# Kernel optimization log

Measured on AMD Instinct MI355X. Metric: run time of the kernel, lower is better.

## Reference

```python
import jax, jax.numpy as jnp
from jax import lax
import numpy as np

B, S, D, H, OUT = 32, 512, 512, 512, 256


def setup_inputs() -> dict:
    key = jax.random.key(0)
    ks = jax.random.split(key, 12)
    sc = 0.05
    return {
        "x": jax.random.normal(ks[0], (B, S, D), jnp.float32),
        "Wf0": jax.random.normal(ks[1], (D + H, H), jnp.float32) * sc,
        "bf0": jax.random.normal(ks[2], (H,), jnp.float32) * sc,
        "Wb0": jax.random.normal(ks[3], (D + H, H), jnp.float32) * sc,
        "bb0": jax.random.normal(ks[4], (H,), jnp.float32) * sc,
        "Wf1": jax.random.normal(ks[5], (3 * H, H), jnp.float32) * sc,
        "bf1": jax.random.normal(ks[6], (H,), jnp.float32) * sc,
        "Wb1": jax.random.normal(ks[7], (3 * H, H), jnp.float32) * sc,
        "bb1": jax.random.normal(ks[8], (H,), jnp.float32) * sc,
        "Wfc": jax.random.normal(ks[9], (2 * H, OUT), jnp.float32) * sc,
        "bfc": jax.random.normal(ks[10], (OUT,), jnp.float32) * sc,
    }


def _direction(xin, W, b, reverse):
    # xin: [B,S,Din]; W: [Din+H, H]. Split into input and hidden parts so the
    # big input projection is one GEMM; only h @ Wh stays in the scan.
    Din = xin.shape[-1]
    Wx, Wh = W[:Din], W[Din:]
    xw = jnp.einsum('bsd,dh->sbh', xin, Wx) + b  # [S,B,H]

    def step(h, xt):
        h = jnp.tanh(xt + h @ Wh)
        return h, h

    h0 = jnp.zeros((xin.shape[0], Wh.shape[1]), xin.dtype)
    h_last, ys = lax.scan(step, h0, xw, reverse=reverse)
    return h_last, jnp.transpose(ys, (1, 0, 2))  # [B,S,H]


def _bilayer(xin, Wf, bf, Wb, bb):
    h_f, out_f = _direction(xin, Wf, bf, reverse=False)
    h_b, out_b = _direction(xin, Wb, bb, reverse=True)
    return jnp.concatenate([out_f, out_b], axis=-1), h_f, h_b


def reference(x, Wf0, bf0, Wb0, bb0, Wf1, bf1, Wb1, bb1, Wfc, bfc):
    y0, hf0, hb0 = _bilayer(x, Wf0, bf0, Wb0, bb0)
    y1, hf1, hb1 = _bilayer(y0, Wf1, bf1, Wb1, bb1)
    seq_repr = jnp.concatenate([hf1, hb1], axis=-1)  # [B, 2H]
    logits = seq_repr @ Wfc + bfc
    final_hf = jnp.stack([hf0, hf1])  # [L,B,H]
    final_hb = jnp.stack([hb0, hb1])
    return logits, final_hf, final_hb
```

## Files before the change

### kernel.cpp

```cpp
#include <hip/hip_runtime.h>


typedef unsigned short u16;
typedef unsigned int u32;
typedef __attribute__((ext_vector_type(8))) short short8;
typedef __attribute__((ext_vector_type(4))) float f32x4;
typedef __attribute__((ext_vector_type(2))) unsigned int u32x2;

#define DEV static __device__ __forceinline__

DEV u16 f2bf(float f) {
  u32 u = __builtin_bit_cast(u32, f);
  u = (u + 0x7fffu + ((u >> 16) & 1u)) >> 16;
  return (u16)u;
}
DEV float bf2f(u16 h) { return __builtin_bit_cast(float, ((u32)h) << 16); }

DEV f32x4 MFMA(short8 a, short8 b, f32x4 c) {
  return __builtin_amdgcn_mfma_f32_16x16x32_bf16(a, b, c, 0, 0, 0);
}

DEV float fast_tanh(float x) {
  float e = exp2f(x * 2.885390082f);
  return 1.0f - 2.0f * __builtin_amdgcn_rcpf(e + 1.0f);
}

DEV short8 ld_b128_coh(const u16* p) {
  short8 r;
  asm volatile("global_load_dwordx4 %0, %1, off sc0 sc1" : "=v"(r) : "v"(p) : "memory");
  return r;
}
DEV short8 ld_b128_l2(const u16* p) {
  short8 r;
  asm volatile("global_load_dwordx4 %0, %1, off sc0" : "=v"(r) : "v"(p) : "memory");
  return r;
}
DEV f32x4 ld_f32x4_vm(const float* p) {
  f32x4 r;
  asm volatile("global_load_dwordx4 %0, %1, off" : "=v"(r) : "v"(p) : "memory");
  return r;
}
DEV u32 ld_u32_coh(const u32* p) {
  u32 r;
  asm volatile("global_load_dword %0, %1, off sc0 sc1\n\ts_waitcnt vmcnt(0)"
               : "=v"(r) : "v"(p) : "memory");
  return r;
}
DEV void st_b64_coh(u16* p, u32x2 v) {
  asm volatile("global_store_dwordx2 %0, %1, off sc0 sc1" :: "v"(p), "v"(v) : "memory");
}
DEV void st_b64_l2(u16* p, u32x2 v) {
  asm volatile("global_store_dwordx2 %0, %1, off sc0" :: "v"(p), "v"(v) : "memory");
}
DEV void st_u32_coh(u32* p, u32 v) {
  asm volatile("global_store_dword %0, %1, off sc0 sc1" :: "v"(p), "v"(v) : "memory");
}
DEV void vm_drain() { asm volatile("s_waitcnt vmcnt(0)" ::: "memory"); }

template<bool LOCAL>
DEV u32 tag_poll(u32* p) {
  u32 r; u32 z = 0;
  if (LOCAL)
    asm volatile("global_atomic_add %0, %1, %2, off sc0\n\ts_waitcnt vmcnt(0)"
                 : "=v"(r) : "v"(p), "v"(z) : "memory");
  else
    asm volatile("global_atomic_add %0, %1, %2, off sc0 sc1\n\ts_waitcnt vmcnt(0)"
                 : "=v"(r) : "v"(p), "v"(z) : "memory");
  return r;
}
template<bool LOCAL>
DEV void tag_post(u32* p) {
  u32 one = 1;
  if (LOCAL)
    asm volatile("global_atomic_add %0, %1, off" :: "v"(p), "v"(one) : "memory");
  else
    asm volatile("global_atomic_add %0, %1, off sc1" :: "v"(p), "v"(one) : "memory");
}

constexpr size_t OFF_CNT  = 0;
constexpr size_t OFF_MB   = 1024;
constexpr size_t OFF_WT0F = 32768;
constexpr size_t NE_WT0   = 512 * 1024;
constexpr size_t SZ_WT0   = NE_WT0 * 2 * 2;
constexpr size_t OFF_WT0B = OFF_WT0F + SZ_WT0;
constexpr size_t OFF_WT1F = OFF_WT0B + SZ_WT0;
constexpr size_t NE_WT1   = 512 * 1536;
constexpr size_t SZ_WT1   = NE_WT1 * 2 * 2;
constexpr size_t OFF_WT1B = OFF_WT1F + SZ_WT1;
constexpr size_t OFF_XWF  = OFF_WT1B + SZ_WT1;
constexpr size_t SZ_XW    = 16384ull * 512 * 4;
constexpr size_t OFF_XWB  = OFF_XWF + SZ_XW;
constexpr size_t OFF_Y0   = OFF_XWB + SZ_XW;
constexpr size_t SZ_Y0    = 16384ull * 1024 * 4;
constexpr size_t OFF_H    = OFF_Y0 + SZ_Y0;

DEV void phase_barrier(u32* c, u32 target) {
  __syncthreads();
  if (threadIdx.x == 0) {
    __hip_atomic_fetch_add(c, 1u, __ATOMIC_RELEASE, __HIP_MEMORY_SCOPE_AGENT);
    int spins = 0;
    while (__hip_atomic_load(c, __ATOMIC_RELAXED, __HIP_MEMORY_SCOPE_AGENT) < target) {
      if (spins < 16) __builtin_amdgcn_s_sleep(32);
      else { __builtin_amdgcn_s_sleep(127); __builtin_amdgcn_s_sleep(127); }
      if (++spins > (1 << 20)) break;
    }
    __builtin_amdgcn_fence(__ATOMIC_ACQUIRE, "agent");
  }
  __syncthreads();
}

DEV void proj_phase(const float* __restrict__ A, bool perm, int bpitch, int bkoff, int K,
                    const u16* __restrict__ wfh, const u16* __restrict__ wfl,
                    const u16* __restrict__ wbh, const u16* __restrict__ wbl,
                    const float* __restrict__ biasF, const float* __restrict__ biasB,
                    float* __restrict__ Cf, float* __restrict__ Cb,
                    u16* aHi, u16* aLo, u16* bHi, u16* bLo) {
  const int tid = threadIdx.x;
  const int l = tid & 63, w = tid >> 6;
  const int lr = l & 15, lk = (l >> 4) * 8;
  const int wm = (w >> 1) * 64, wn = (w & 1) * 64;
  for (int t = blockIdx.x; t < 1024; t += 256) {
    const int dir = t >> 9, tile = t & 511;
    const int mbase = (tile >> 2) * 128, nbase = (tile & 3) * 128;
    const u16* bh_src = dir ? wbh : wfh;
    const u16* bl_src = dir ? wbl : wfl;
    const float* bias = dir ? biasB : biasF;
    float* C = dir ? Cb : Cf;
    f32x4 acc[4][4] = {};
    for (int kk = 0; kk < K; kk += 32) {
      {
        const int row = tid >> 1, half = tid & 1;
        const int r = mbase + row;
        const int srcRow = perm ? (((r & 31) << 9) + (r >> 5)) : r;
        const float* ap = A + (size_t)srcRow * K + kk + half * 16;
        f32x4 q0 = *(const f32x4*)(ap + 0);
        f32x4 q1 = *(const f32x4*)(ap + 4);
        f32x4 q2 = *(const f32x4*)(ap + 8);
        f32x4 q3 = *(const f32x4*)(ap + 12);
        short8 h0, l0, h1, l1;
        #pragma unroll
        for (int e = 0; e < 4; ++e) {
          { float v = q0[e]; u16 hv = f2bf(v); h0[e]   = (short)hv; l0[e]   = (short)f2bf(v - bf2f(hv)); }
          { float v = q1[e]; u16 hv = f2bf(v); h0[e+4] = (short)hv; l0[e+4] = (short)f2bf(v - bf2f(hv)); }
          { float v = q2[e]; u16 hv = f2bf(v); h1[e]   = (short)hv; l1[e]   = (short)f2bf(v - bf2f(hv)); }
          { float v = q3[e]; u16 hv = f2bf(v); h1[e+4] = (short)hv; l1[e+4] = (short)f2bf(v - bf2f(hv)); }
        }
        const int o = row * 40 + half * 16;
        *(short8*)&aHi[o] = h0; *(short8*)&aHi[o + 8] = h1;
        *(short8*)&aLo[o] = l0; *(short8*)&aLo[o + 8] = l1;
        const size_t bo = (size_t)(nbase + row) * bpitch + bkoff + kk + half * 16;
        *(short8*)&bHi[o]     = *(const short8*)&bh_src[bo];
        *(short8*)&bHi[o + 8] = *(const short8*)&bh_src[bo + 8];
        *(short8*)&bLo[o]     = *(const short8*)&bl_src[bo];
        *(short8*)&bLo[o + 8] = *(const short8*)&bl_src[bo + 8];
      }
      __syncthreads();
      short8 afh[4], afl[4], bfh[4], bfl[4];
      #pragma unroll
      for (int i = 0; i < 4; ++i) {
        afh[i] = *(short8*)&aHi[(wm + i * 16 + lr) * 40 + lk];
        afl[i] = *(short8*)&aLo[(wm + i * 16 + lr) * 40 + lk];
        bfh[i] = *(short8*)&bHi[(wn + i * 16 + lr) * 40 + lk];
        bfl[i] = *(short8*)&bLo[(wn + i * 16 + lr) * 40 + lk];
      }
      #pragma unroll
      for (int i = 0; i < 4; ++i)
        #pragma unroll
        for (int j = 0; j < 4; ++j) {
          acc[i][j] = MFMA(afh[i], bfh[j], acc[i][j]);
          acc[i][j] = MFMA(afh[i], bfl[j], acc[i][j]);
          acc[i][j] = MFMA(afl[i], bfh[j], acc[i][j]);
        }
      __syncthreads();
    }
    #pragma unroll
    for (int i = 0; i < 4; ++i)
      #pragma unroll
      for (int j = 0; j < 4; ++j) {
        const int gcol = nbase + wn + j * 16 + lr;
        const float bv = bias[gcol];
        #pragma unroll
        for (int rr = 0; rr < 4; ++rr) {
          const int grow = mbase + wm + i * 16 + (l >> 4) * 4 + rr;
          C[(size_t)grow * 512 + gcol] = acc[i][j][rr] + bv;
        }
      }
  }
}

template<bool LOCAL>
DEV void recurrence(bool fwd, const float* __restrict__ xw,
                    const u16* __restrict__ wtHi, const u16* __restrict__ wtLo,
                    int wpitch, int wkoff,
                    u16* __restrict__ hHi, u16* __restrict__ hLo,
                    float* __restrict__ y0, int ycol0,
                    u32* mb, int wgslot, float* red) {
  const int tid = threadIdx.x;
  const int l = tid & 63, w = tid >> 6;
  const int lr = l & 15, lk4 = l >> 4;
  const int c0 = wgslot * 64;
  short8 wfh[4][4], wfl[4][4];
  #pragma unroll
  for (int ct = 0; ct < 4; ++ct)
    #pragma unroll
    for (int ks = 0; ks < 4; ++ks) {
      const size_t o = (size_t)(c0 + ct * 16 + lr) * wpitch + wkoff + w * 128 + ks * 32 + lk4 * 8;
      wfh[ct][ks] = *(const short8*)&wtHi[o];
      wfl[ct][ks] = *(const short8*)&wtLo[o];
    }
  const int frow = (w & 1) * 16 + lr;
  const int fcb  = c0 + (w >> 1) * 16 + lk4 * 4;
  const u32 mySlot = (u32)(wgslot * 4 + w);
  u32* pollp = mb + wgslot * 64 + (l & 31);
  int budget = 1 << 22;
  for (int t = 0; t < 512; ++t) {
    const int s = fwd ? t : (511 - t);
    const float* xwp = xw + (size_t)(s * 32 + frow) * 512 + fcb;
    f32x4 xwA = ld_f32x4_vm(xwp);
    f32x4 xwB = ld_f32x4_vm(xwp + 32);
    if (t) {
      for (;;) {
        u32 v = tag_poll<LOCAL>(pollp);
        if (__all((int)(v >= (u32)t))) break;
        if (--budget < 0) break;
      }
    }
    const u16* hh = hHi + (t & 1) * 16384;
    const u16* hl = hLo + (t & 1) * 16384;
    u16* nhh = hHi + ((t & 1) ^ 1) * 16384;
    u16* nhl = hLo + ((t & 1) ^ 1) * 16384;
    short8 hfh0[4], hfl0[4], hfh1[4], hfl1[4];
    #pragma unroll
    for (int g = 0; g < 4; ++g) {
      const int k = w * 128 + g * 32 + lk4 * 8;
      if (LOCAL) {
        hfh0[g] = ld_b128_l2(&hh[lr * 512 + k]);
        hfl0[g] = ld_b128_l2(&hl[lr * 512 + k]);
        hfh1[g] = ld_b128_l2(&hh[(16 + lr) * 512 + k]);
        hfl1[g] = ld_b128_l2(&hl[(16 + lr) * 512 + k]);
      } else {
        hfh0[g] = ld_b128_coh(&hh[lr * 512 + k]);
        hfl0[g] = ld_b128_coh(&hl[lr * 512 + k]);
        hfh1[g] = ld_b128_coh(&hh[(16 + lr) * 512 + k]);
        hfl1[g] = ld_b128_coh(&hl[(16 + lr) * 512 + k]);
      }
    }
    f32x4 acc[4][2] = {};
    #pragma unroll
    for (int g = 0; g < 4; ++g) {
      if (g == 0)      asm volatile("s_waitcnt vmcnt(12)" ::: "memory");
      else if (g == 1) asm volatile("s_waitcnt vmcnt(8)"  ::: "memory");
      else if (g == 2) asm volatile("s_waitcnt vmcnt(4)"  ::: "memory");
      else             asm volatile("s_waitcnt vmcnt(0)"  ::: "memory");
      __builtin_amdgcn_sched_barrier(0);
      #pragma unroll
      for (int ct = 0; ct < 4; ++ct) {
        acc[ct][0] = MFMA(wfh[ct][g], hfh0[g], acc[ct][0]);
        acc[ct][0] = MFMA(wfh[ct][g], hfl0[g], acc[ct][0]);
        acc[ct][0] = MFMA(wfl[ct][g], hfh0[g], acc[ct][0]);
        acc[ct][1] = MFMA(wfh[ct][g], hfh1[g], acc[ct][1]);
        acc[ct][1] = MFMA(wfh[ct][g], hfl1[g], acc[ct][1]);
        acc[ct][1] = MFMA(wfl[ct][g], hfh1[g], acc[ct][1]);
      }
    }
    #pragma unroll
    for (int ct = 0; ct < 4; ++ct)
      #pragma unroll
      for (int rh = 0; rh < 2; ++rh)
        *(f32x4*)&red[((w * 8 + ct * 2 + rh) * 64 + l) * 4] = acc[ct][rh];
    __syncthreads();
    f32x4 finA = xwA, finB = xwB;
    #pragma unroll
    for (int wp = 0; wp < 4; ++wp) {
      finA += *(const f32x4*)&red[((wp * 8 + w) * 64 + l) * 4];
      finB += *(const f32x4*)&red[((wp * 8 + w + 4) * 64 + l) * 4];
    }
    f32x4 tA, tB;
    #pragma unroll
    for (int rr = 0; rr < 4; ++rr) { tA[rr] = fast_tanh(finA[rr]); tB[rr] = fast_tanh(finB[rr]); }
    u32x2 hwA, lwA, hwB, lwB;
    {
      u16 hv[8], lv[8];
      #pragma unroll
      for (int i = 0; i < 4; ++i) {
        hv[i] = f2bf(tA[i]); lv[i] = f2bf(tA[i] - bf2f(hv[i]));
        hv[4 + i] = f2bf(tB[i]); lv[4 + i] = f2bf(tB[i] - bf2f(hv[4 + i]));
      }
      hwA[0] = (u32)hv[0] | ((u32)hv[1] << 16); hwA[1] = (u32)hv[2] | ((u32)hv[3] << 16);
      lwA[0] = (u32)lv[0] | ((u32)lv[1] << 16); lwA[1] = (u32)lv[2] | ((u32)lv[3] << 16);
      hwB[0] = (u32)hv[4] | ((u32)hv[5] << 16); hwB[1] = (u32)hv[6] | ((u32)hv[7] << 16);
      lwB[0] = (u32)lv[4] | ((u32)lv[5] << 16); lwB[1] = (u32)lv[6] | ((u32)lv[7] << 16);
    }
    if (LOCAL) {
      st_b64_l2(&nhh[frow * 512 + fcb], hwA);
      st_b64_l2(&nhl[frow * 512 + fcb], lwA);
      st_b64_l2(&nhh[frow * 512 + fcb + 32], hwB);
      st_b64_l2(&nhl[frow * 512 + fcb + 32], lwB);
    } else {
      st_b64_coh(&nhh[frow * 512 + fcb], hwA);
      st_b64_coh(&nhl[frow * 512 + fcb], lwA);
      st_b64_coh(&nhh[frow * 512 + fcb + 32], hwB);
      st_b64_coh(&nhl[frow * 512 + fcb + 32], lwB);
    }
    vm_drain();
    if (l < 8) tag_post<LOCAL>(mb + l * 64 + mySlot);
    if (y0) {
      *(f32x4*)&y0[(size_t)(s * 32 + frow) * 1024 + ycol0 + fcb] = tA;
      *(f32x4*)&y0[(size_t)(s * 32 + frow) * 1024 + ycol0 + fcb + 32] = tB;
    }
  }
}

__global__ void rnn_init(u32* c) {
  #pragma unroll
  for (int i = 0; i < 8; ++i) c[threadIdx.x * 8 + i] = 0;
}

__global__ __launch_bounds__(256, 1) void rnn_main(
    const float* __restrict__ x,
    const float* __restrict__ Wf0, const float* __restrict__ bf0,
    const float* __restrict__ Wb0, const float* __restrict__ bb0,
    const float* __restrict__ Wf1, const float* __restrict__ bf1,
    const float* __restrict__ Wb1, const float* __restrict__ bb1,
    const float* __restrict__ Wfc, const float* __restrict__ bfc,
    float* __restrict__ out, char* __restrict__ ws) {
  __shared__ __align__(16) u16 lds[20480];
  u16* aHi = lds; u16* aLo = lds + 5120; u16* bHi = lds + 10240; u16* bLo = lds + 15360;
  float* red = (float*)lds;
  __shared__ u32 sh_xcd, sh_slot, sh_el;

  u32* cnt = (u32*)(ws + OFF_CNT);
  u32* mbase = (u32*)(ws + OFF_MB);
  u16* wt0f_hi = (u16*)(ws + OFF_WT0F); u16* wt0f_lo = wt0f_hi + NE_WT0;
  u16* wt0b_hi = (u16*)(ws + OFF_WT0B); u16* wt0b_lo = wt0b_hi + NE_WT0;
  u16* wt1f_hi = (u16*)(ws + OFF_WT1F); u16* wt1f_lo = wt1f_hi + NE_WT1;
  u16* wt1b_hi = (u16*)(ws + OFF_WT1B); u16* wt1b_lo = wt1b_hi + NE_WT1;
  float* xwf = (float*)(ws + OFF_XWF);
  float* xwb = (float*)(ws + OFF_XWB);
  float* y0  = (float*)(ws + OFF_Y0);
  u16* hb = (u16*)(ws + OFF_H);

  const int gtid = blockIdx.x * 256 + threadIdx.x;
  const int bid = blockIdx.x;

  if (threadIdx.x == 0) {
    u32 xcd;
    asm volatile("s_getreg_b32 %0, hwreg(HW_REG_XCC_ID)" : "=s"(xcd));
    xcd &= 7u;
    sh_xcd = xcd;
    sh_slot = __hip_atomic_fetch_add(&cnt[128 + xcd], 1u, __ATOMIC_RELAXED,
                                     __HIP_MEMORY_SCOPE_AGENT);
  }
  __syncthreads();
  const u32 myXcd = sh_xcd, mySlotIdx = sh_slot;

  for (u32 j = gtid; j < (u32)NE_WT0; j += 65536u) {
    const u32 n = j >> 10, r = j & 1023;
    float v = Wf0[(size_t)r * 512 + n];
    u16 hv = f2bf(v); wt0f_hi[j] = hv; wt0f_lo[j] = f2bf(v - bf2f(hv));
    v = Wb0[(size_t)r * 512 + n];
    hv = f2bf(v); wt0b_hi[j] = hv; wt0b_lo[j] = f2bf(v - bf2f(hv));
  }
  for (u32 j = gtid; j < (u32)NE_WT1; j += 65536u) {
    const u32 n = j / 1536u, r = j - n * 1536u;
    float v = Wf1[(size_t)r * 512 + n];
    u16 hv = f2bf(v); wt1f_hi[j] = hv; wt1f_lo[j] = f2bf(v - bf2f(hv));
    v = Wb1[(size_t)r * 512 + n];
    hv = f2bf(v); wt1b_hi[j] = hv; wt1b_lo[j] = f2bf(v - bf2f(hv));
  }
  for (u32 j = gtid; j < 131072u; j += 65536u) ((u32*)hb)[j] = 0;

  u32 ep = 0;
  phase_barrier(cnt, (++ep) * 256);

  if (bid == 0 && threadIdx.x == 0) {
    u32 cv[8];
    for (int i = 0; i < 8; ++i) cv[i] = ld_u32_coh(&cnt[128 + i]);
    int fwdX = 0;
    for (int i = 1; i < 8; ++i) if (cv[i] > cv[fwdX]) fwdX = i;
    int bwdX = (fwdX == 0) ? 1 : 0;
    for (int i = 0; i < 8; ++i) if (i != fwdX && cv[i] > cv[bwdX]) bwdX = i;
    u32 ok = (cv[fwdX] >= 8 && cv[bwdX] >= 8) ? 1u : 0u;
    st_u32_coh(&cnt[160], (u32)fwdX | ((u32)bwdX << 4) | (ok << 8));
    vm_drain();
  }
  phase_barrier(cnt, (++ep) * 256);
  if (threadIdx.x == 0) sh_el = ld_u32_coh(&cnt[160]);
  __syncthreads();
  const u32 el = sh_el;
  const int fwdX = (int)(el & 15), bwdX = (int)((el >> 4) & 15);
  const bool useLocal = ((el >> 8) & 1) != 0;

  bool rf, rb; int slot;
  if (useLocal) {
    rf = ((int)myXcd == fwdX) && (mySlotIdx < 8);
    rb = ((int)myXcd == bwdX) && (mySlotIdx < 8);
    slot = (int)mySlotIdx;
  } else {
    rf = bid < 8;
    rb = bid >= 8 && bid < 16;
    slot = bid & 7;
  }

  proj_phase(x, true, 1024, 0, 512, wt0f_hi, wt0f_lo, wt0b_hi, wt0b_lo,
             bf0, bb0, xwf, xwb, aHi, aLo, bHi, bLo);
  phase_barrier(cnt, (++ep) * 256);

  if (rf) {
    if (useLocal) recurrence<true >(true,  xwf, wt0f_hi, wt0f_lo, 1024, 512,
                    hb + 0 * 65536, hb + 0 * 65536 + 32768, y0, 0,   mbase,        slot, red);
    else          recurrence<false>(true,  xwf, wt0f_hi, wt0f_lo, 1024, 512,
                    hb + 0 * 65536, hb + 0 * 65536 + 32768, y0, 0,   mbase,        slot, red);
  } else if (rb) {
    if (useLocal) recurrence<true >(false, xwb, wt0b_hi, wt0b_lo, 1024, 512,
                    hb + 1 * 65536, hb + 1 * 65536 + 32768, y0, 512, mbase + 1024, slot, red);
    else          recurrence<false>(false, xwb, wt0b_hi, wt0b_lo, 1024, 512,
                    hb + 1 * 65536, hb + 1 * 65536 + 32768, y0, 512, mbase + 1024, slot, red);
  }
  phase_barrier(cnt, (++ep) * 256);

  proj_phase(y0, false, 1536, 0, 1024, wt1f_hi, wt1f_lo, wt1b_hi, wt1b_lo,
             bf1, bb1, xwf, xwb, aHi, aLo, bHi, bLo);
  phase_barrier(cnt, (++ep) * 256);

  if (rf) {
    if (useLocal) recurrence<true >(true,  xwf, wt1f_hi, wt1f_lo, 1536, 1024,
                    hb + 2 * 65536, hb + 2 * 65536 + 32768, nullptr, 0, mbase + 2048, slot, red);
    else          recurrence<false>(true,  xwf, wt1f_hi, wt1f_lo, 1536, 1024,
                    hb + 2 * 65536, hb + 2 * 65536 + 32768, nullptr, 0, mbase + 2048, slot, red);
  } else if (rb) {
    if (useLocal) recurrence<true >(false, xwb, wt1b_hi, wt1b_lo, 1536, 1024,
                    hb + 3 * 65536, hb + 3 * 65536 + 32768, nullptr, 0, mbase + 3072, slot, red);
    else          recurrence<false>(false, xwb, wt1b_hi, wt1b_lo, 1536, 1024,
                    hb + 3 * 65536, hb + 3 * 65536 + 32768, nullptr, 0, mbase + 3072, slot, red);
  }
  phase_barrier(cnt, (++ep) * 256);

  {
    const int i = gtid;
    const int dl = i >> 14, idx = i & 16383;
    const u16* hh = hb + dl * 65536;
    const u16* hl = hh + 32768;
    const float v = bf2f(hh[idx]) + bf2f(hl[idx]);
    const int base = 8192 + ((dl & 1) ? 32768 : 0) + ((dl >> 1) ? 16384 : 0);
    out[base + idx] = v;
  }
  if (bid < 32) {
    const int gid = gtid;
    const int b = gid >> 8, o = gid & 255;
    const u16* f1h = hb + 2 * 65536; const u16* f1l = f1h + 32768;
    const u16* b1h = hb + 3 * 65536; const u16* b1l = b1h + 32768;
    float a = bfc[o];
    for (int k = 0; k < 512; ++k)
      a += (bf2f(f1h[b * 512 + k]) + bf2f(f1l[b * 512 + k])) * Wfc[(size_t)k * 256 + o];
    for (int k = 0; k < 512; ++k)
      a += (bf2f(b1h[b * 512 + k]) + bf2f(b1l[b * 512 + k])) * Wfc[(size_t)(512 + k) * 256 + o];
    out[gid] = a;
  }
}

extern "C" void kernel_launch(void* const* d_in, const int* in_sizes, int n_in,
                              void* d_out, int out_size, void* d_ws, size_t ws_size,
                              hipStream_t stream) {
  (void)in_sizes; (void)n_in; (void)out_size; (void)ws_size;
  const float* x   = (const float*)d_in[0];
  const float* Wf0 = (const float*)d_in[1];
  const float* bf0 = (const float*)d_in[2];
  const float* Wb0 = (const float*)d_in[3];
  const float* bb0 = (const float*)d_in[4];
  const float* Wf1 = (const float*)d_in[5];
  const float* bf1 = (const float*)d_in[6];
  const float* Wb1 = (const float*)d_in[7];
  const float* bb1 = (const float*)d_in[8];
  const float* Wfc = (const float*)d_in[9];
  const float* bfc = (const float*)d_in[10];
  rnn_init<<<1, 1024, 0, stream>>>((u32*)d_ws);
  rnn_main<<<256, 256, 0, stream>>>(x, Wf0, bf0, Wb0, bb0, Wf1, bf1, Wb1, bb1,
                                    Wfc, bfc, (float*)d_out, (char*)d_ws);
}
```

Measured before the change: 4.842 ms.

## Split recurrence by output tiles per wave, removing LDS K-reduction

Each wave in the recurrence now owns a 16-row by 32-column output tile over the full K dimension, instead of a K-slice of the whole 32x64 block. That removes the LDS partial-sum reduction and its mid-step barrier. Step signalling also changes from per-wave tag slots polled by 32 lanes to one per-workgroup counter polled by a single lane, posted after a workgroup barrier. The cost is twice as many weight registers per wave and only two long dependent MFMA accumulation chains, which may expose MFMA latency or add register pressure.

```diff
diff --git a/kernel.cpp b/kernel.cpp
--- a/kernel.cpp
+++ b/kernel.cpp
@@ -194,34 +194,36 @@
                     int wpitch, int wkoff,
                     u16* __restrict__ hHi, u16* __restrict__ hLo,
                     float* __restrict__ y0, int ycol0,
-                    u32* mb, int wgslot, float* red) {
+                    u32* mb, int wgslot) {
   const int tid = threadIdx.x;
   const int l = tid & 63, w = tid >> 6;
   const int lr = l & 15, lk4 = l >> 4;
-  const int c0 = wgslot * 64;
-  short8 wfh[4][4], wfl[4][4];
+  const int rh = w & 1, cp = w >> 1;
+  const int c0 = wgslot * 64 + cp * 32;
+  const int frow = rh * 16 + lr;
+  const int fcb  = c0 + lk4 * 4;
+  short8 wfh[2][16], wfl[2][16];
   #pragma unroll
-  for (int ct = 0; ct < 4; ++ct)
+  for (int ct = 0; ct < 2; ++ct)
     #pragma unroll
-    for (int ks = 0; ks < 4; ++ks) {
-      const size_t o = (size_t)(c0 + ct * 16 + lr) * wpitch + wkoff + w * 128 + ks * 32 + lk4 * 8;
+    for (int ks = 0; ks < 16; ++ks) {
+      const size_t o = (size_t)(c0 + ct * 16 + lr) * wpitch + wkoff + ks * 32 + lk4 * 8;
       wfh[ct][ks] = *(const short8*)&wtHi[o];
       wfl[ct][ks] = *(const short8*)&wtLo[o];
     }
-  const int frow = (w & 1) * 16 + lr;
-  const int fcb  = c0 + (w >> 1) * 16 + lk4 * 4;
-  const u32 mySlot = (u32)(wgslot * 4 + w);
-  u32* pollp = mb + wgslot * 64 + (l & 31);
+  u32* myCnt = mb + wgslot * 32;
   int budget = 1 << 22;
   for (int t = 0; t < 512; ++t) {
     const int s = fwd ? t : (511 - t);
     const float* xwp = xw + (size_t)(s * 32 + frow) * 512 + fcb;
     f32x4 xwA = ld_f32x4_vm(xwp);
-    f32x4 xwB = ld_f32x4_vm(xwp + 32);
+    f32x4 xwB = ld_f32x4_vm(xwp + 16);
     if (t) {
+      const u32 tgt = 8u * (u32)t;
       for (;;) {
-        u32 v = tag_poll<LOCAL>(pollp);
-        if (__all((int)(v >= (u32)t))) break;
+        u32 okl = 1;
+        if (l == 0) okl = (tag_poll<LOCAL>(myCnt) >= tgt) ? 1u : 0u;
+        if (__all((int)okl)) break;
         if (--budget < 0) break;
       }
     }
@@ -229,55 +231,35 @@
     const u16* hl = hLo + (t & 1) * 16384;
     u16* nhh = hHi + ((t & 1) ^ 1) * 16384;
     u16* nhl = hLo + ((t & 1) ^ 1) * 16384;
-    short8 hfh0[4], hfl0[4], hfh1[4], hfl1[4];
+    short8 hfh[16], hfl[16];
     #pragma unroll
-    for (int g = 0; g < 4; ++g) {
-      const int k = w * 128 + g * 32 + lk4 * 8;
-      if (LOCAL) {
-        hfh0[g] = ld_b128_l2(&hh[lr * 512 + k]);
-        hfl0[g] = ld_b128_l2(&hl[lr * 512 + k]);
-        hfh1[g] = ld_b128_l2(&hh[(16 + lr) * 512 + k]);
-        hfl1[g] = ld_b128_l2(&hl[(16 + lr) * 512 + k]);
-      } else {
-        hfh0[g] = ld_b128_coh(&hh[lr * 512 + k]);
-        hfl0[g] = ld_b128_coh(&hl[lr * 512 + k]);
-        hfh1[g] = ld_b128_coh(&hh[(16 + lr) * 512 + k]);
-        hfl1[g] = ld_b128_coh(&hl[(16 + lr) * 512 + k]);
-      }
-    }
-    f32x4 acc[4][2] = {};
+    for (int ks = 0; ks < 16; ++ks) {
+      const u16* ph = &hh[(size_t)frow * 512 + ks * 32 + lk4 * 8];
+      const u16* pl = &hl[(size_t)frow * 512 + ks * 32 + lk4 * 8];
+      if (LOCAL) { hfh[ks] = ld_b128_l2(ph);  hfl[ks] = ld_b128_l2(pl); }
+      else       { hfh[ks] = ld_b128_coh(ph); hfl[ks] = ld_b128_coh(pl); }
+    }
+    f32x4 acc[2] = {};
     #pragma unroll
-    for (int g = 0; g < 4; ++g) {
-      if (g == 0)      asm volatile("s_waitcnt vmcnt(12)" ::: "memory");
-      else if (g == 1) asm volatile("s_waitcnt vmcnt(8)"  ::: "memory");
-      else if (g == 2) asm volatile("s_waitcnt vmcnt(4)"  ::: "memory");
-      else             asm volatile("s_waitcnt vmcnt(0)"  ::: "memory");
-      __builtin_amdgcn_sched_barrier(0);
+    for (int ks = 0; ks < 16; ++ks) {
+      if (ks == 0)       asm volatile("s_waitcnt vmcnt(24)" ::: "memory");
+      else if (ks == 4)  asm volatile("s_waitcnt vmcnt(16)" ::: "memory");
+      else if (ks == 8)  asm volatile("s_waitcnt vmcnt(8)"  ::: "memory");
+      else if (ks == 12) asm volatile("s_waitcnt vmcnt(0)"  ::: "memory");
+      if ((ks & 3) == 0) __builtin_amdgcn_sched_barrier(0);
       #pragma unroll
-      for (int ct = 0; ct < 4; ++ct) {
-        acc[ct][0] = MFMA(wfh[ct][g], hfh0[g], acc[ct][0]);
-        acc[ct][0] = MFMA(wfh[ct][g], hfl0[g], acc[ct][0]);
-        acc[ct][0] = MFMA(wfl[ct][g], hfh0[g], acc[ct][0]);
-        acc[ct][1] = MFMA(wfh[ct][g], hfh1[g], acc[ct][1]);
-        acc[ct][1] = MFMA(wfh[ct][g], hfl1[g], acc[ct][1]);
-        acc[ct][1] = MFMA(wfl[ct][g], hfh1[g], acc[ct][1]);
-      }
-    }
-    #pragma unroll
-    for (int ct = 0; ct < 4; ++ct)
-      #pragma unroll
-      for (int rh = 0; rh < 2; ++rh)
-        *(f32x4*)&red[((w * 8 + ct * 2 + rh) * 64 + l) * 4] = acc[ct][rh];
-    __syncthreads();
-    f32x4 finA = xwA, finB = xwB;
-    #pragma unroll
-    for (int wp = 0; wp < 4; ++wp) {
-      finA += *(const f32x4*)&red[((wp * 8 + w) * 64 + l) * 4];
-      finB += *(const f32x4*)&red[((wp * 8 + w + 4) * 64 + l) * 4];
+      for (int ct = 0; ct < 2; ++ct) {
+        acc[ct] = MFMA(wfh[ct][ks], hfh[ks], acc[ct]);
+        acc[ct] = MFMA(wfh[ct][ks], hfl[ks], acc[ct]);
+        acc[ct] = MFMA(wfl[ct][ks], hfh[ks], acc[ct]);
+      }
     }
     f32x4 tA, tB;
     #pragma unroll
-    for (int rr = 0; rr < 4; ++rr) { tA[rr] = fast_tanh(finA[rr]); tB[rr] = fast_tanh(finB[rr]); }
+    for (int rr = 0; rr < 4; ++rr) {
+      tA[rr] = fast_tanh(xwA[rr] + acc[0][rr]);
+      tB[rr] = fast_tanh(xwB[rr] + acc[1][rr]);
+    }
     u32x2 hwA, lwA, hwB, lwB;
     {
       u16 hv[8], lv[8];
@@ -294,19 +276,20 @@
     if (LOCAL) {
       st_b64_l2(&nhh[frow * 512 + fcb], hwA);
       st_b64_l2(&nhl[frow * 512 + fcb], lwA);
-      st_b64_l2(&nhh[frow * 512 + fcb + 32], hwB);
-      st_b64_l2(&nhl[frow * 512 + fcb + 32], lwB);
+      st_b64_l2(&nhh[frow * 512 + fcb + 16], hwB);
+      st_b64_l2(&nhl[frow * 512 + fcb + 16], lwB);
     } else {
       st_b64_coh(&nhh[frow * 512 + fcb], hwA);
       st_b64_coh(&nhl[frow * 512 + fcb], lwA);
-      st_b64_coh(&nhh[frow * 512 + fcb + 32], hwB);
-      st_b64_coh(&nhl[frow * 512 + fcb + 32], lwB);
+      st_b64_coh(&nhh[frow * 512 + fcb + 16], hwB);
+      st_b64_coh(&nhl[frow * 512 + fcb + 16], lwB);
     }
     vm_drain();
-    if (l < 8) tag_post<LOCAL>(mb + l * 64 + mySlot);
+    __syncthreads();
+    if (tid < 8) tag_post<LOCAL>(mb + tid * 32);
     if (y0) {
       *(f32x4*)&y0[(size_t)(s * 32 + frow) * 1024 + ycol0 + fcb] = tA;
-      *(f32x4*)&y0[(size_t)(s * 32 + frow) * 1024 + ycol0 + fcb + 32] = tB;
+      *(f32x4*)&y0[(size_t)(s * 32 + frow) * 1024 + ycol0 + fcb + 16] = tB;
     }
   }
 }
@@ -326,7 +309,6 @@
     float* __restrict__ out, char* __restrict__ ws) {
   __shared__ __align__(16) u16 lds[20480];
   u16* aHi = lds; u16* aLo = lds + 5120; u16* bHi = lds + 10240; u16* bLo = lds + 15360;
-  float* red = (float*)lds;
   __shared__ u32 sh_xcd, sh_slot, sh_el;
 
   u32* cnt = (u32*)(ws + OFF_CNT);
@@ -408,14 +390,14 @@
 
   if (rf) {
     if (useLocal) recurrence<true >(true,  xwf, wt0f_hi, wt0f_lo, 1024, 512,
-                    hb + 0 * 65536, hb + 0 * 65536 + 32768, y0, 0,   mbase,        slot, red);
+                    hb + 0 * 65536, hb + 0 * 65536 + 32768, y0, 0,   mbase,        slot);
     else          recurrence<false>(true,  xwf, wt0f_hi, wt0f_lo, 1024, 512,
-                    hb + 0 * 65536, hb + 0 * 65536 + 32768, y0, 0,   mbase,        slot, red);
+                    hb + 0 * 65536, hb + 0 * 65536 + 32768, y0, 0,   mbase,        slot);
   } else if (rb) {
     if (useLocal) recurrence<true >(false, xwb, wt0b_hi, wt0b_lo, 1024, 512,
-                    hb + 1 * 65536, hb + 1 * 65536 + 32768, y0, 512, mbase + 1024, slot, red);
+                    hb + 1 * 65536, hb + 1 * 65536 + 32768, y0, 512, mbase + 1024, slot);
     else          recurrence<false>(false, xwb, wt0b_hi, wt0b_lo, 1024, 512,
-                    hb + 1 * 65536, hb + 1 * 65536 + 32768, y0, 512, mbase + 1024, slot, red);
+                    hb + 1 * 65536, hb + 1 * 65536 + 32768, y0, 512, mbase + 1024, slot);
   }
   phase_barrier(cnt, (++ep) * 256);
 
@@ -425,14 +407,14 @@
 
   if (rf) {
     if (useLocal) recurrence<true >(true,  xwf, wt1f_hi, wt1f_lo, 1536, 1024,
-                    hb + 2 * 65536, hb + 2 * 65536 + 32768, nullptr, 0, mbase + 2048, slot, red);
+                    hb + 2 * 65536, hb + 2 * 65536 + 32768, nullptr, 0, mbase + 2048, slot);
     else          recurrence<false>(true,  xwf, wt1f_hi, wt1f_lo, 1536, 1024,
-                    hb + 2 * 65536, hb + 2 * 65536 + 32768, nullptr, 0, mbase + 2048, slot, red);
+                    hb + 2 * 65536, hb + 2 * 65536 + 32768, nullptr, 0, mbase + 2048, slot);
   } else if (rb) {
     if (useLocal) recurrence<true >(false, xwb, wt1b_hi, wt1b_lo, 1536, 1024,
-                    hb + 3 * 65536, hb + 3 * 65536 + 32768, nullptr, 0, mbase + 3072, slot, red);
+                    hb + 3 * 65536, hb + 3 * 65536 + 32768, nullptr, 0, mbase + 3072, slot);
     else          recurrence<false>(false, xwb, wt1b_hi, wt1b_lo, 1536, 1024,
-                    hb + 3 * 65536, hb + 3 * 65536 + 32768, nullptr, 0, mbase + 3072, slot, red);
+                    hb + 3 * 65536, hb + 3 * 65536 + 32768, nullptr, 0, mbase + 3072, slot);
   }
   phase_barrier(cnt, (++ep) * 256);
 
```

Result: slower. 5.935 ms (+22.6%).
